# Performance work log

Measured on AMD Instinct MI355X. Metric: run time of the kernel, lower is better.

Reference implementation:

```python
import jax, jax.numpy as jnp
import numpy as np

N = 1048576   # nodes (1024x1024 fluid grid)
E = 8388608   # edges (avg degree 8)
IDX_NODE_X, IDX_NODE_Y = 0, 1
IDX_EDGE_X, IDX_EDGE_Y = 0, 1


def setup_inputs() -> dict:
    key = jax.random.key(0)
    ks = jax.random.split(key, 9)
    v_x = jax.random.normal(ks[0], (N, 2), jnp.float32)
    v_prev_x = jax.random.normal(ks[1], (N, 2), jnp.float32)
    p_x = jax.random.normal(ks[2], (N, 1), jnp.float32)
    p_prev_x = jax.random.normal(ks[3], (N, 1), jnp.float32)
    rho_x = jax.random.normal(ks[4], (N, 1), jnp.float32)
    rho_prev_x = jax.random.normal(ks[5], (N, 1), jnp.float32)
    edge_attr = jax.random.normal(ks[6], (E, 2), jnp.float32)
    # mimic grid finite-difference sparsity: ~half the entries of each
    # direction column are exactly zero, exercising the != 0 edge masking
    keep = jax.random.bernoulli(ks[7], 0.5, (E, 2))
    edge_attr = jnp.where(keep, edge_attr, 0.0)
    edge_index = jax.random.randint(ks[8], (2, E), 0, N, dtype=jnp.int64)
    return dict(
        v_x=v_x, v_prev_x=v_prev_x, p_x=p_x, p_prev_x=p_prev_x,
        rho_x=rho_x, rho_prev_x=rho_prev_x,
        M=jnp.float32(1.0), eta=jnp.float32(1.0), zeta=jnp.float32(1.0),
        dt=jnp.float32(0.01), edge_attr=edge_attr, edge_index=edge_index,
    )


def _spatial_derivative(x, src, dst, edge_attr, mask, idx_node, idx_edge, n):
    """Gather-compute-scatter finite difference: scatter-mean of
    (x[dst, idx_node] - x[src, idx_node]) / edge_attr[:, idx_edge]
    over the masked edge subset, aggregated at the source node."""
    diff = x[dst, idx_node] - x[src, idx_node]                  # [E]
    denom = jnp.where(mask, edge_attr[:, idx_edge], 1.0)        # avoid /0 on masked-out edges
    contrib = jnp.where(mask, diff / denom, 0.0)                # [E]
    sums = jax.ops.segment_sum(contrib, src, num_segments=n)    # [N]
    cnt = jax.ops.segment_sum(mask.astype(x.dtype), src, num_segments=n)
    return sums / jnp.maximum(cnt, 1.0)                         # [N]


def reference(v_x, v_prev_x, p_x, p_prev_x, rho_x, rho_prev_x, M, eta, zeta, dt, edge_attr, edge_index):
    n = v_x.shape[0]
    src, dst = edge_index[0], edge_index[1]
    vp = v_x * p_x                                  # [N,2] * [N,1] -> [N,2]
    mask_x = edge_attr[:, IDX_NODE_X] != 0          # edges with x-offset
    mask_y = edge_attr[:, IDX_NODE_Y] != 0          # edges with y-offset
    d_x = _spatial_derivative(vp, src, dst, edge_attr, mask_x, IDX_NODE_X, IDX_EDGE_X, n)
    d_y = _spatial_derivative(vp, src, dst, edge_attr, mask_y, IDX_NODE_Y, IDX_EDGE_Y, n)
    loss_continuity = (d_x + d_y)[:, None] + (p_x - p_prev_x) / dt   # [N,1]
    return loss_continuity
```

## Files before the change

kernel.cpp:

```cpp
#include <hip/hip_runtime.h>
#include <hip/hip_fp16.h>


#define NPB      2048
#define NPB_LOG  11
#define NBUCK_MAX 512
#define CE       4096
#define CB       1024
#define EPT      4
#define CCAP     4608
#define MAXCHUNK 2048
#define K_OFF    1073741824.0

typedef unsigned long long ull;


__global__ void node_pre_fast(const float2* __restrict__ v,
                              const float* __restrict__ p,
                              float2* __restrict__ vpf,
                              __half2* __restrict__ vph,
                              double2* __restrict__ side,
                              int* __restrict__ oflow, int N) {
    int i = blockIdx.x * blockDim.x + threadIdx.x;
    int stride = gridDim.x * blockDim.x;
    for (; i < N; i += stride) {
        float2 vi = v[i];
        float pi = p[i];
        float2 vp = make_float2(vi.x * pi, vi.y * pi);
        vpf[i] = vp;
        vph[i] = __float22half2_rn(vp);
        side[i] = make_double2(0.0, 0.0);
    }
    if (blockIdx.x == 0 && threadIdx.x == 0) *oflow = 0;
}

__device__ __forceinline__ void route_rec(uint2 r, int k, size_t rb, int slot,
                                          uint2* __restrict__ recs,
                                          const float2* __restrict__ vpf,
                                          double2* __restrict__ side,
                                          int* __restrict__ oflow) {
    if (slot < CCAP) { recs[rb + slot] = r; return; }
    unsigned sl = r.x & (NPB - 1u);
    bool diry = (r.x >> 11) & 1u;
    int d = (int)(r.x >> 12);
    float a = __uint_as_float(r.y);
    int s = k * NPB + (int)sl;
    float2 vpd = vpf[d], vs = vpf[s];
    float c = (diry ? vpd.y - vs.y : vpd.x - vs.x) / a;
    unsafeAtomicAdd(diry ? &side[s].y : &side[s].x, (double)c + K_OFF);
    atomicOr(oflow, 1);
}

__global__ __launch_bounds__(CB) void chunk_sort(
        const float2* __restrict__ ea,
        const int* __restrict__ src_idx,
        const int* __restrict__ dst_idx,
        const float2* __restrict__ vpf,
        uint2* __restrict__ recs,
        unsigned short* __restrict__ off_mat,
        unsigned short* __restrict__ cnt_mat,
        double2* __restrict__ side,
        int* __restrict__ oflow,
        int nbuck, int E) {
    __shared__ uint2 stage[CCAP];
    __shared__ int hist[NBUCK_MAX];
    __shared__ int tl[NBUCK_MAX];
    __shared__ int cur[NBUCK_MAX];
    int c = blockIdx.x, t = threadIdx.x;
    int e0 = c * CE;

    uint2 R0[EPT], R1[EPT];
    int K[EPT], NR[EPT];
#pragma unroll
    for (int i = 0; i < EPT; ++i) {
        int e = e0 + i * CB + t;
        NR[i] = 0; K[i] = 0;
        if (e < E) {
            float2 a = ea[e];
            bool mx = (a.x != 0.f);
            bool my = (a.y != 0.f);
            if (mx || my) {
                int s = src_idx[e];
                int d = dst_idx[e];
                K[i] = s >> NPB_LOG;
                unsigned sl = (unsigned)(s & (NPB - 1));
                unsigned dm = (unsigned)d << 12;
                NR[i] = (int)mx + (int)my;
                uint2 rx = make_uint2(sl | dm, __float_as_uint(a.x));
                uint2 ry = make_uint2(sl | 0x800u | dm, __float_as_uint(a.y));
                R0[i] = mx ? rx : ry;
                R1[i] = ry;
            }
        }
    }
    if (t < nbuck) hist[t] = 0;
    __syncthreads();
#pragma unroll
    for (int i = 0; i < EPT; ++i)
        if (NR[i]) atomicAdd(&hist[K[i]], NR[i]);
    __syncthreads();
    if (t < nbuck) tl[t] = hist[t];
    __syncthreads();
    for (int off = 1; off < NBUCK_MAX; off <<= 1) {
        int x = 0;
        if (t < nbuck && t >= off) x = tl[t - off];
        __syncthreads();
        if (t < nbuck) tl[t] += x;
        __syncthreads();
    }
    int total = tl[nbuck - 1];
    if (t < nbuck) {
        int excl = tl[t] - hist[t];
        cur[t] = excl;
        off_mat[(size_t)c * nbuck + t] = (unsigned short)excl;
        cnt_mat[(size_t)c * nbuck + t] = (unsigned short)hist[t];
    }
    __syncthreads();
    size_t rb = (size_t)c * CCAP;
    if (total <= CCAP) {
#pragma unroll
        for (int i = 0; i < EPT; ++i)
            if (NR[i]) {
                int slot = atomicAdd(&cur[K[i]], NR[i]);
                stage[slot] = R0[i];
                if (NR[i] == 2) stage[slot + 1] = R1[i];
            }
        __syncthreads();
        for (int j = t; j < total; j += CB) recs[rb + j] = stage[j];
    } else {
#pragma unroll
        for (int i = 0; i < EPT; ++i)
            if (NR[i]) {
                int slot = atomicAdd(&cur[K[i]], NR[i]);
                route_rec(R0[i], K[i], rb, slot, recs, vpf, side, oflow);
                if (NR[i] == 2) route_rec(R1[i], K[i], rb, slot + 1, recs, vpf, side, oflow);
            }
    }
}

__global__ __launch_bounds__(1024) void bucket_reduce(
        const uint2* __restrict__ recs,
        const unsigned short* __restrict__ off_mat,
        const unsigned short* __restrict__ cnt_mat,
        const float2* __restrict__ vpf,
        const __half2* __restrict__ vph,
        const double2* __restrict__ side,
        const int* __restrict__ oflow,
        const float* __restrict__ p,
        const float* __restrict__ p_prev,
        const float* __restrict__ dt_ptr,
        float* __restrict__ out,
        int nchunk, int nbuck, int N) {
    __shared__ float2 vps[NPB];
    __shared__ double2 acc[NPB];
    __shared__ int glen[MAXCHUNK];
    __shared__ int goff[MAXCHUNK];
    __shared__ int s_of;
    int k = blockIdx.x, t = threadIdx.x;
    int g0 = k * NPB;
    for (int i = t; i < NPB; i += 1024) {
        int g = g0 + i;
        vps[i] = (g < N) ? vpf[g] : make_float2(0.f, 0.f);
        acc[i] = make_double2(0.0, 0.0);
    }
    if (t == 0) s_of = *oflow;
    for (int c = t; c < MAXCHUNK; c += 1024) {
        int len = 0, off = 0;
        if (c < nchunk) {
            off = __builtin_nontemporal_load(&off_mat[(size_t)c * nbuck + k]);
            int cnt = __builtin_nontemporal_load(&cnt_mat[(size_t)c * nbuck + k]);
            len = min(cnt, max(0, CCAP - off));
        }
        goff[c] = off;
        glen[c] = len;
    }
    __syncthreads();
    for (int off = 1; off < MAXCHUNK; off <<= 1) {
        int i0 = t, i1 = t + 1024;
        int x0 = (i0 >= off) ? glen[i0 - off] : 0;
        int x1 = glen[i1 - off];
        __syncthreads();
        glen[i0] += x0;
        glen[i1] += x1;
        __syncthreads();
    }
    int total = glen[MAXCHUNK - 1];
    const ull* recs64 = (const ull*)recs;
    for (int idx = t; idx < total; idx += 1024) {
        int lo = 0, hi = nchunk - 1;
        while (lo < hi) {
            int mid = (lo + hi) >> 1;
            if (glen[mid] > idx) hi = mid; else lo = mid + 1;
        }
        int pre = lo ? glen[lo - 1] : 0;
        ull rv = __builtin_nontemporal_load(
            &recs64[(size_t)lo * CCAP + goff[lo] + (idx - pre)]);
        unsigned m = (unsigned)rv;
        float a = __uint_as_float((unsigned)(rv >> 32));
        int sl = (int)(m & (NPB - 1u));
        bool diry = (m >> 11) & 1u;
        int d = (int)(m >> 12);
        float2 vpd = __half22float2(vph[d]);
        float2 vs = vps[sl];
        float c = (diry ? vpd.y - vs.y : vpd.x - vs.x) / a;
        unsafeAtomicAdd(diry ? &acc[sl].y : &acc[sl].x, (double)c + K_OFF);
    }
    __syncthreads();
    float inv_dt = 1.0f / dt_ptr[0];
    for (int i = t; i < NPB; i += 1024) {
        int g = g0 + i;
        if (g < N) {
            double2 A = acc[i];
            if (s_of) {
                double2 S = side[g];
                A.x += S.x; A.y += S.y;
            }
            double cx = rint(A.x * (1.0 / K_OFF));
            double sx = A.x - cx * K_OFF;
            double cy = rint(A.y * (1.0 / K_OFF));
            double sy = A.y - cy * K_OFF;
            out[g] = (float)(sx / fmax(cx, 1.0)) + (float)(sy / fmax(cy, 1.0))
                   + (p[g] - p_prev[g]) * inv_dt;
        }
    }
}


__global__ void fb_node_pre(const float2* __restrict__ v,
                            const float* __restrict__ p,
                            float2* __restrict__ vp,
                            double2* __restrict__ acc, int N) {
    int i = blockIdx.x * blockDim.x + threadIdx.x;
    int stride = gridDim.x * blockDim.x;
    for (; i < N; i += stride) {
        float2 vi = v[i];
        float pi = p[i];
        vp[i] = make_float2(vi.x * pi, vi.y * pi);
        acc[i] = make_double2(0.0, 0.0);
    }
}

__global__ void fb_edge_scatter(const float2* __restrict__ vp,
                                const float2* __restrict__ ea,
                                const int* __restrict__ src_idx,
                                const int* __restrict__ dst_idx,
                                double2* __restrict__ acc, int E) {
    int e = blockIdx.x * blockDim.x + threadIdx.x;
    if (e >= E) return;
    float2 a = ea[e];
    bool mx = (a.x != 0.f);
    bool my = (a.y != 0.f);
    if (!mx && !my) return;
    int s = src_idx[e];
    int d = dst_idx[e];
    float2 vs = vp[s];
    float2 vd = vp[d];
    double* basep = (double*)&acc[s];
    if (mx) unsafeAtomicAdd(basep + 0, (double)((vd.x - vs.x) / a.x) + K_OFF);
    if (my) unsafeAtomicAdd(basep + 1, (double)((vd.y - vs.y) / a.y) + K_OFF);
}

__global__ void fb_node_final(const double2* __restrict__ acc,
                              const float* __restrict__ p,
                              const float* __restrict__ p_prev,
                              const float* __restrict__ dt_ptr,
                              float* __restrict__ out, int N) {
    int i = blockIdx.x * blockDim.x + threadIdx.x;
    int stride = gridDim.x * blockDim.x;
    float inv_dt = 1.0f / dt_ptr[0];
    for (; i < N; i += stride) {
        double2 A = acc[i];
        double cx = rint(A.x * (1.0 / K_OFF));
        double sx = A.x - cx * K_OFF;
        double cy = rint(A.y * (1.0 / K_OFF));
        double sy = A.y - cy * K_OFF;
        out[i] = (float)(sx / fmax(cx, 1.0)) + (float)(sy / fmax(cy, 1.0))
               + (p[i] - p_prev[i]) * inv_dt;
    }
}


extern "C" void kernel_launch(void* const* d_in, const int* in_sizes, int n_in,
                              void* d_out, int out_size, void* d_ws, size_t ws_size,
                              hipStream_t stream) {
    const float2* v_x    = (const float2*)d_in[0];
    const float*  p_x    = (const float*)d_in[2];
    const float*  p_prev = (const float*)d_in[3];
    const float*  dt     = (const float*)d_in[9];
    const float2* ea     = (const float2*)d_in[10];
    const int*    eidx   = (const int*)d_in[11];

    const int N = in_sizes[2];
    const int E = in_sizes[10] / 2;
    const int* src_idx = eidx;
    const int* dst_idx = eidx + E;

    const int nbuck  = (N + NPB - 1) >> NPB_LOG;
    const int nchunk = (E + CE - 1) / CE;

    char* w = (char*)d_ws;
    float2*  vpf     = (float2*)w;    w += (size_t)N * sizeof(float2);
    __half2* vph     = (__half2*)w;   w += (size_t)N * sizeof(__half2);
    double2* side    = (double2*)w;   w += (size_t)N * sizeof(double2);
    int*     oflow   = (int*)w;       w += 16;
    unsigned short* off_mat = (unsigned short*)w;  w += (size_t)nchunk * nbuck * sizeof(unsigned short);
    unsigned short* cnt_mat = (unsigned short*)w;  w += (size_t)nchunk * nbuck * sizeof(unsigned short);
    w = (char*)(((uintptr_t)w + 15) & ~(uintptr_t)15);
    uint2*   recs    = (uint2*)w;     w += (size_t)nchunk * CCAP * sizeof(uint2);
    size_t need_fast = (size_t)(w - (char*)d_ws);

    if (nbuck <= NBUCK_MAX && nchunk <= MAXCHUNK && N <= (1 << 20)
        && ws_size >= need_fast) {
        node_pre_fast<<<2048, 256, 0, stream>>>(v_x, p_x, vpf, vph, side, oflow, N);
        chunk_sort<<<nchunk, CB, 0, stream>>>(ea, src_idx, dst_idx, vpf, recs,
                                              off_mat, cnt_mat, side, oflow,
                                              nbuck, E);
        bucket_reduce<<<nbuck, 1024, 0, stream>>>(recs, off_mat, cnt_mat,
                                                  vpf, vph, side, oflow,
                                                  p_x, p_prev, dt,
                                                  (float*)d_out, nchunk, nbuck, N);
    } else {
        float2*  fvp  = (float2*)d_ws;
        double2* facc = (double2*)((char*)d_ws + (size_t)N * sizeof(float2));
        fb_node_pre<<<2048, 256, 0, stream>>>(v_x, p_x, fvp, facc, N);
        fb_edge_scatter<<<(E + 255) / 256, 256, 0, stream>>>(
            fvp, ea, src_idx, dst_idx, facc, E);
        fb_node_final<<<2048, 256, 0, stream>>>(
            facc, p_x, p_prev, dt, (float*)d_out, N);
    }
}
```

Measured before the change: 152.9 us.

## Drop float vp buffer and replace per-record binary search with hint table

The node precompute no longer writes a full-precision v*p array. The overflow path and the bucket_reduce preload now recompute v*p from v and p directly, which removes an 8 MB write and its later reads. In bucket_reduce, a shared hint table of chunk indices is built once for every 8th record position, so each thread does a short linear advance instead of a full binary search over chunk prefix sums. The cost is some extra shared memory and an added synchronisation.

```diff
diff --git a/kernel.cpp b/kernel.cpp
--- a/kernel.cpp
+++ b/kernel.cpp
@@ -10,6 +10,7 @@
 #define EPT      4
 #define CCAP     4608
 #define MAXCHUNK 2048
+#define NHINT    4096
 #define K_OFF    1073741824.0
 
 typedef unsigned long long ull;
@@ -17,7 +18,6 @@
 
 __global__ void node_pre_fast(const float2* __restrict__ v,
                               const float* __restrict__ p,
-                              float2* __restrict__ vpf,
                               __half2* __restrict__ vph,
                               double2* __restrict__ side,
                               int* __restrict__ oflow, int N) {
@@ -26,9 +26,7 @@
     for (; i < N; i += stride) {
         float2 vi = v[i];
         float pi = p[i];
-        float2 vp = make_float2(vi.x * pi, vi.y * pi);
-        vpf[i] = vp;
-        vph[i] = __float22half2_rn(vp);
+        vph[i] = __float22half2_rn(make_float2(vi.x * pi, vi.y * pi));
         side[i] = make_double2(0.0, 0.0);
     }
     if (blockIdx.x == 0 && threadIdx.x == 0) *oflow = 0;
@@ -36,7 +34,8 @@
 
 __device__ __forceinline__ void route_rec(uint2 r, int k, size_t rb, int slot,
                                           uint2* __restrict__ recs,
-                                          const float2* __restrict__ vpf,
+                                          const float2* __restrict__ v,
+                                          const float* __restrict__ p,
                                           double2* __restrict__ side,
                                           int* __restrict__ oflow) {
     if (slot < CCAP) { recs[rb + slot] = r; return; }
@@ -45,8 +44,9 @@
     int d = (int)(r.x >> 12);
     float a = __uint_as_float(r.y);
     int s = k * NPB + (int)sl;
-    float2 vpd = vpf[d], vs = vpf[s];
-    float c = (diry ? vpd.y - vs.y : vpd.x - vs.x) / a;
+    float2 vd = v[d], vs = v[s];
+    float pd = p[d], ps = p[s];
+    float c = (diry ? vd.y * pd - vs.y * ps : vd.x * pd - vs.x * ps) / a;
     unsafeAtomicAdd(diry ? &side[s].y : &side[s].x, (double)c + K_OFF);
     atomicOr(oflow, 1);
 }
@@ -55,7 +55,8 @@
         const float2* __restrict__ ea,
         const int* __restrict__ src_idx,
         const int* __restrict__ dst_idx,
-        const float2* __restrict__ vpf,
+        const float2* __restrict__ v,
+        const float* __restrict__ p,
         uint2* __restrict__ recs,
         unsigned short* __restrict__ off_mat,
         unsigned short* __restrict__ cnt_mat,
@@ -132,8 +133,8 @@
         for (int i = 0; i < EPT; ++i)
             if (NR[i]) {
                 int slot = atomicAdd(&cur[K[i]], NR[i]);
-                route_rec(R0[i], K[i], rb, slot, recs, vpf, side, oflow);
-                if (NR[i] == 2) route_rec(R1[i], K[i], rb, slot + 1, recs, vpf, side, oflow);
+                route_rec(R0[i], K[i], rb, slot, recs, v, p, side, oflow);
+                if (NR[i] == 2) route_rec(R1[i], K[i], rb, slot + 1, recs, v, p, side, oflow);
             }
     }
 }
@@ -142,11 +143,11 @@
         const uint2* __restrict__ recs,
         const unsigned short* __restrict__ off_mat,
         const unsigned short* __restrict__ cnt_mat,
-        const float2* __restrict__ vpf,
+        const float2* __restrict__ v,
+        const float* __restrict__ p,
         const __half2* __restrict__ vph,
         const double2* __restrict__ side,
         const int* __restrict__ oflow,
-        const float* __restrict__ p,
         const float* __restrict__ p_prev,
         const float* __restrict__ dt_ptr,
         float* __restrict__ out,
@@ -155,12 +156,15 @@
     __shared__ double2 acc[NPB];
     __shared__ int glen[MAXCHUNK];
     __shared__ int goff[MAXCHUNK];
+    __shared__ unsigned short hint[NHINT];
     __shared__ int s_of;
     int k = blockIdx.x, t = threadIdx.x;
     int g0 = k * NPB;
     for (int i = t; i < NPB; i += 1024) {
         int g = g0 + i;
-        vps[i] = (g < N) ? vpf[g] : make_float2(0.f, 0.f);
+        float2 vi = (g < N) ? v[g] : make_float2(0.f, 0.f);
+        float pi = (g < N) ? p[g] : 0.f;
+        vps[i] = make_float2(vi.x * pi, vi.y * pi);
         acc[i] = make_double2(0.0, 0.0);
     }
     if (t == 0) s_of = *oflow;
@@ -185,16 +189,35 @@
         __syncthreads();
     }
     int total = glen[MAXCHUNK - 1];
-    const ull* recs64 = (const ull*)recs;
-    for (int idx = t; idx < total; idx += 1024) {
+    int nh = min((total + 7) >> 3, NHINT);
+    for (int j = t; j < nh; j += 1024) {
+        int target = j << 3;
         int lo = 0, hi = nchunk - 1;
         while (lo < hi) {
             int mid = (lo + hi) >> 1;
-            if (glen[mid] > idx) hi = mid; else lo = mid + 1;
-        }
-        int pre = lo ? glen[lo - 1] : 0;
+            if (glen[mid] > target) hi = mid; else lo = mid + 1;
+        }
+        hint[j] = (unsigned short)lo;
+    }
+    __syncthreads();
+    const ull* recs64 = (const ull*)recs;
+    for (int idx = t; idx < total; idx += 1024) {
+        int j = idx >> 3;
+        int cur;
+        if (j < NHINT) {
+            cur = hint[j];
+        } else {
+            int lo = 0, hi = nchunk - 1;
+            while (lo < hi) {
+                int mid = (lo + hi) >> 1;
+                if (glen[mid] > idx) hi = mid; else lo = mid + 1;
+            }
+            cur = lo;
+        }
+        while (glen[cur] <= idx) ++cur;
+        int pre = cur ? glen[cur - 1] : 0;
         ull rv = __builtin_nontemporal_load(
-            &recs64[(size_t)lo * CCAP + goff[lo] + (idx - pre)]);
+            &recs64[(size_t)cur * CCAP + goff[cur] + (idx - pre)]);
         unsigned m = (unsigned)rv;
         float a = __uint_as_float((unsigned)(rv >> 32));
         int sl = (int)(m & (NPB - 1u));
@@ -299,7 +322,6 @@
     const int nchunk = (E + CE - 1) / CE;
 
     char* w = (char*)d_ws;
-    float2*  vpf     = (float2*)w;    w += (size_t)N * sizeof(float2);
     __half2* vph     = (__half2*)w;   w += (size_t)N * sizeof(__half2);
     double2* side    = (double2*)w;   w += (size_t)N * sizeof(double2);
     int*     oflow   = (int*)w;       w += 16;
@@ -311,13 +333,13 @@
 
     if (nbuck <= NBUCK_MAX && nchunk <= MAXCHUNK && N <= (1 << 20)
         && ws_size >= need_fast) {
-        node_pre_fast<<<2048, 256, 0, stream>>>(v_x, p_x, vpf, vph, side, oflow, N);
-        chunk_sort<<<nchunk, CB, 0, stream>>>(ea, src_idx, dst_idx, vpf, recs,
-                                              off_mat, cnt_mat, side, oflow,
-                                              nbuck, E);
+        node_pre_fast<<<2048, 256, 0, stream>>>(v_x, p_x, vph, side, oflow, N);
+        chunk_sort<<<nchunk, CB, 0, stream>>>(ea, src_idx, dst_idx, v_x, p_x,
+                                              recs, off_mat, cnt_mat, side,
+                                              oflow, nbuck, E);
         bucket_reduce<<<nbuck, 1024, 0, stream>>>(recs, off_mat, cnt_mat,
-                                                  vpf, vph, side, oflow,
-                                                  p_x, p_prev, dt,
+                                                  v_x, p_x, vph, side, oflow,
+                                                  p_prev, dt,
                                                   (float*)d_out, nchunk, nbuck, N);
     } else {
         float2*  fvp  = (float2*)d_ws;
```

Result: no change. 153.7 us (+0.5%).
